# Optimization experiments

Hardware: AMD Instinct MI355X
Metric: run time of the kernel (lower is better)

Reference implementation:

```python
import jax, jax.numpy as jnp
import numpy as np

S, B, IN, H, NLAYERS = 2048, 1024, 4, 4, 6  # 3 stacked nn.LSTM modules x num_layers=2 each


def setup_inputs() -> dict:
    key = jax.random.key(0)
    ks = jax.random.split(key, 7)
    scale = 1.0 / np.sqrt(H)  # PyTorch LSTM init range
    return {
        "x": jax.random.normal(ks[0], (S, B, IN), jnp.float32),
        "w_ih": jax.random.uniform(ks[1], (NLAYERS, 4 * H, H), jnp.float32, -scale, scale),
        "w_hh": jax.random.uniform(ks[2], (NLAYERS, 4 * H, H), jnp.float32, -scale, scale),
        "b_ih": jax.random.uniform(ks[3], (NLAYERS, 4 * H), jnp.float32, -scale, scale),
        "b_hh": jax.random.uniform(ks[4], (NLAYERS, 4 * H), jnp.float32, -scale, scale),
        "reg_w": jax.random.uniform(ks[5], (1, H), jnp.float32, -scale, scale),
        "reg_b": jax.random.uniform(ks[6], (1,), jnp.float32, -scale, scale),
    }


def _lstm_layer(x, w_ih, w_hh, b_ih, b_hh):
    # x: [S, B, H_in]; PyTorch gate order: input, forget, cell(g), output
    b = x.shape[1]
    pre = jnp.einsum('sbi,gi->sbg', x, w_ih) + b_ih + b_hh  # [S, B, 4H], input projection hoisted out of scan

    def step(carry, p):
        h, c = carry
        gates = p + h @ w_hh.T
        i, f, g, o = jnp.split(gates, 4, axis=-1)
        c = jax.nn.sigmoid(f) * c + jax.nn.sigmoid(i) * jnp.tanh(g)
        h = jax.nn.sigmoid(o) * jnpat(c) if False else jax.nn.sigmoid(o) * jnp.tanh(c)
        return (h, c), h

    h0 = jnp.zeros((b, H), x.dtype)
    (_, _), ys = jax.lax.scan(step, (h0, h0), pre)
    return ys  # [S, B, H]


def reference(x, w_ih, w_hh, b_ih, b_hh, reg_w, reg_b):
    # 6 stacked LSTM layers (lstm1: layers 0-1, lstm2: 2-3, lstm3: 4-5).
    # Dropout (p=0.02) between layers and dropout3 are identity in eval mode.
    y = x
    for l in range(NLAYERS):
        y = _lstm_layer(y, w_ih[l], w_hh[l], b_ih[l], b_hh[l])
    out = jnp.einsum('sbh,oh->sbo', y, reg_w) + reg_b  # linear head, [S, B, 1]
    return out
```

## Files before the change

### kernel.cpp

```cpp
#include <hip/hip_runtime.h>

#define S_LEN  2048
#define BATCH  1024
#define NL     6
#define CH     16

typedef float f32x2 __attribute__((ext_vector_type(2)));

__device__ __forceinline__ float fexp2(float x) { return __builtin_amdgcn_exp2f(x); }
__device__ __forceinline__ float frcp(float x)  { return __builtin_amdgcn_rcpf(x); }

template <int CTRL>
__device__ __forceinline__ float dppf(float v) {
    return __int_as_float(__builtin_amdgcn_update_dpp(
        0, __float_as_int(v), CTRL, 0xF, 0xF, true));
}
__device__ __forceinline__ float bpermf(int addr, float v) {
    return __int_as_float(__builtin_amdgcn_ds_bpermute(addr, __float_as_int(v)));
}
__device__ __forceinline__ float swz4(float v) {
    return __int_as_float(__builtin_amdgcn_ds_swizzle(__float_as_int(v), 0x101F));
}
__device__ __forceinline__ f32x2 pkfma(f32x2 a, f32x2 b, f32x2 c) {
    f32x2 d;
    asm("v_pk_fma_f32 %0, %1, %2, %3" : "=v"(d) : "v"(a), "v"(b), "v"(c));
    return d;
}

__global__ __launch_bounds__(64, 1) void lstm_wavepipe(
    const float* __restrict__ x, const float* __restrict__ w_ih,
    const float* __restrict__ w_hh, const float* __restrict__ b_ih,
    const float* __restrict__ b_hh, const float* __restrict__ reg_w,
    const float* __restrict__ reg_b, float* __restrict__ out) {
    const int lane = threadIdx.x;
    const int L    = lane >> 3;
    const int q    = lane & 7;
    const int u    = q >> 1;
    const bool pOdd = (lane & 1);
    const int b    = blockIdx.x;
    const bool isFeeder = (L == 7);
    const bool isOut    = (lane == 48);

    const float KGc = -2.885390082f;
    const float KIc = -1.442695041f;

    f32x2 A1[4], A2[4], PB;
    if (L < NL) {
        const int gLo = pOdd ? 2 : 0;
        const int gHi = pOdd ? 3 : 1;
        const float klo = pOdd ? KGc : KIc;
        const float khi = KIc;
        const int rowLo = L * 16 + gLo * 4 + u;
        const int rowHi = L * 16 + gHi * 4 + u;
#pragma unroll
        for (int m = 0; m < 4; ++m) {
            const int cm = u ^ m;
            f32x2 a1, a2;
            a1.x = w_hh[rowLo * 4 + cm] * klo;
            a1.y = w_ih[rowHi * 4 + cm] * khi;
            a2.x = w_hh[rowHi * 4 + cm] * khi;
            a2.y = w_ih[rowLo * 4 + cm] * klo;
            A1[m] = a1; A2[m] = a2;
        }
        PB.x = (b_ih[rowLo] + b_hh[rowLo]) * klo;
        PB.y = (b_ih[rowHi] + b_hh[rowHi]) * khi;
    } else if (L == 6) {
#pragma unroll
        for (int m = 0; m < 4; ++m) {
            f32x2 a1; a1.x = 0.0f; a1.y = reg_w[u ^ m];
            A1[m] = a1;
            f32x2 a2; a2.x = 0.0f; a2.y = 0.0f;
            A2[m] = a2;
        }
        PB.x = 0.0f; PB.y = reg_b[0];
    } else {
#pragma unroll
        for (int m = 0; m < 4; ++m) {
            f32x2 z; z.x = 0.0f; z.y = 0.0f;
            A1[m] = z; A2[m] = z;
        }
        PB.x = 0.0f; PB.y = 0.0f;
    }
    const float aLo = pOdd ? 2.0f : 1.0f;
    const float bLo = pOdd ? -1.0f : 0.0f;
    f32x2 Z2; Z2.x = 0.0f; Z2.y = 0.0f;

    const int src   = (lane >= 8) ? (lane - 8) : (lane + 56);
    const int addrA = src << 2;
    const int addrB = (src ^ 4) << 2;

    float c = 0.0f;
    float bufP[CH], bufQ[CH], su[CH];
    const uint32_t xcol = (uint32_t)(b * 4 + u);
    uint32_t wi = xcol;
#pragma unroll
    for (int uu = 0; uu < CH; ++uu) { bufP[uu] = x[wi]; wi += 4096; }

    f32x2 P0, P2;
    {
        const float h0 = isFeeder ? bufP[0] : 0.0f;
        P0.x = h0; P0.y = bpermf(addrA, h0);
        P2.x = swz4(h0); P2.y = bpermf(addrB, h0);
    }

#define STEP(u_, NXV_, MASKF_) do {                                            \
    f32x2 P1, P3;                                                              \
    P1.x = dppf<0x4E>(P0.x); P1.y = dppf<0x4E>(P0.y);                          \
    P3.x = dppf<0x4E>(P2.x); P3.y = dppf<0x4E>(P2.y);                          \
    f32x2 C1 = pkfma(A1[0], P0, PB);                                           \
    f32x2 C2 = pkfma(A2[0], P0, Z2);                                           \
    C1 = pkfma(A1[1], P1, C1); C2 = pkfma(A2[1], P1, C2);                      \
    C1 = pkfma(A1[2], P2, C1); C2 = pkfma(A2[2], P2, C2);                      \
    C1 = pkfma(A1[3], P3, C1); C2 = pkfma(A2[3], P3, C2);                      \
    const float gLo = C1.x + C2.y;                                             \
    const float gHi = C1.y + C2.x;                                             \
    const float rA = frcp(1.0f + fexp2(gLo));                                  \
    const float rB = frcp(1.0f + fexp2(gHi));                                  \
    const float sA = fmaf(aLo, rA, bLo);       \
    const float tg = dppf<0xB1>(sA);                    \
    const float so = dppf<0xB1>(rB);                    \
    const float cn = fmaf(rB, c, sA * tg);             \
    const float th = fmaf(2.0f, frcp(1.0f + fexp2(cn * KGc)), -1.0f);          \
    const float hn = so * th;                                                  \
    const float hx = dppf<0xB1>(hn);                     \
    float hsel = pOdd ? hx : hn;                                               \
    if (MASKF_) {                                                              \
        const bool act = (u_ >= L);                    \
        c = act ? cn : c;                                                      \
        hsel = act ? hsel : P0.x;                                              \
    } else { c = cn; }                                                         \
    su[u_] = gHi;                                 \
    const float hpub = isFeeder ? (NXV_) : hsel;                               \
    P0.x = hpub;                                                               \
    P0.y = bpermf(addrA, hpub);                     \
    P2.x = swz4(hpub);                              \
    P2.y = bpermf(addrB, hpub);                     \
} while (0)

#define RUN_CHUNK(cc_, cur_, nxt_, MASKF_, PREFM_, GUARDF_, NSTEPS_) do {      \
    if ((PREFM_) == 1) {                                                       \
        _Pragma("unroll")                                                      \
        for (int uu = 0; uu < CH; ++uu) { nxt_[uu] = x[wi]; wi += 4096; }      \
    } else if ((PREFM_) == 2) {                                                \
        const float xl = x[2047u * 4096u + xcol];                              \
        _Pragma("unroll")                                                      \
        for (int uu = 0; uu < CH; ++uu) nxt_[uu] = xl;                         \
    }                                                                          \
    _Pragma("unroll")                                                          \
    for (int uu = 0; uu < (NSTEPS_); ++uu) {                                   \
        if (uu < CH - 1) STEP(uu, cur_[uu + 1], MASKF_);                       \
        else             STEP(uu, nxt_[0],      MASKF_);                       \
    }                                                                          \
    if (isOut) {                                                               \
        const int base = (cc_) * CH - 6;       \
        _Pragma("unroll")                                                      \
        for (int uu = 0; uu < (NSTEPS_); ++uu) {                               \
            const int t = base + uu;                                           \
            if (!(GUARDF_) || ((t >= 0) && (t < S_LEN)))                       \
                out[(size_t)t * BATCH + b] = su[uu];                           \
        }                                                                      \
    }                                                                          \
} while (0)

    RUN_CHUNK(0, bufP, bufQ, 1, 1, 1, CH);
#pragma unroll 1
    for (int cc = 1; cc < 127; cc += 2) {
        RUN_CHUNK(cc,     bufQ, bufP, 0, 1, 0, CH);
        RUN_CHUNK(cc + 1, bufP, bufQ, 0, 1, 0, CH);
    }
    RUN_CHUNK(127, bufQ, bufP, 0, 2, 0, CH);
    RUN_CHUNK(128, bufP, bufQ, 0, 0, 0, 6);
#undef RUN_CHUNK
#undef STEP
}

extern "C" void kernel_launch(void* const* d_in, const int* in_sizes, int n_in,
                              void* d_out, int out_size, void* d_ws, size_t ws_size,
                              hipStream_t stream) {
    const float* x     = (const float*)d_in[0];
    const float* w_ih  = (const float*)d_in[1];
    const float* w_hh  = (const float*)d_in[2];
    const float* b_ih  = (const float*)d_in[3];
    const float* b_hh  = (const float*)d_in[4];
    const float* reg_w = (const float*)d_in[5];
    const float* reg_b = (const float*)d_in[6];
    float* out = (float*)d_out;

    dim3 grid(BATCH);
    dim3 block(64);
    hipLaunchKernelGGL(lstm_wavepipe, grid, block, 0, stream, x, w_ih, w_hh,
                       b_ih, b_hh, reg_w, reg_b, out);
}
```

Measured before the change: 340.6 us.

## Deepen LSTM wavefront pipeline to two-step inter-layer lag with split h/c publish

Restructures the per-step recurrence so that each layer's hidden state reaches the next layer through one bpermute with a two-step lag, instead of a single-step lag that needed two bpermutes and a swizzle on the critical path. Own-layer h feeds the recurrence directly, and the cross-lane values for the next step are prefetched one step ahead. The KGc scale is folded into the cell state. The pipeline latency per layer doubles (12 drain steps instead of 6), and the output index offset and masking are adjusted to match. The aim is to shorten the serial dependency chain per timestep at the cost of a longer fill and drain.

```diff
diff --git a/kernel.cpp b/kernel.cpp
--- a/kernel.cpp
+++ b/kernel.cpp
@@ -81,30 +81,30 @@
         }
         PB.x = 0.0f; PB.y = 0.0f;
     }
-    const float aLo = pOdd ? 2.0f : 1.0f;
+    const float aLo = pOdd ? 2.0f : KGc;
     const float bLo = pOdd ? -1.0f : 0.0f;
     f32x2 Z2; Z2.x = 0.0f; Z2.y = 0.0f;
 
-    const int src   = (lane >= 8) ? (lane - 8) : (lane + 56);
-    const int addrA = src << 2;
-    const int addrB = (src ^ 4) << 2;
+    const int addrA = (((lane >= 8) ? (lane - 8) : (lane + 56)) << 2);
 
-    float c = 0.0f;
+    float h = 0.0f, cp = 0.0f;
     float bufP[CH], bufQ[CH], su[CH];
     const uint32_t xcol = (uint32_t)(b * 4 + u);
     uint32_t wi = xcol;
 #pragma unroll
     for (int uu = 0; uu < CH; ++uu) { bufP[uu] = x[wi]; wi += 4096; }
 
-    f32x2 P0, P2;
-    {
-        const float h0 = isFeeder ? bufP[0] : 0.0f;
-        P0.x = h0; P0.y = bpermf(addrA, h0);
-        P2.x = swz4(h0); P2.y = bpermf(addrB, h0);
-    }
+    const float pub0 = isFeeder ? bufP[0] : 0.0f;
+    const float pub1 = isFeeder ? bufP[1] : 0.0f;
+    float hupC = bpermf(addrA, pub0);
+    float hupN = bpermf(addrA, pub1);
+    float P2xC = 0.0f;
+    float P2yC = swz4(hupC);
 
 #define STEP(u_, NXV_, MASKF_) do {                                            \
-    f32x2 P1, P3;                                                              \
+    f32x2 P0, P1, P2, P3;                                                      \
+    P0.x = h;    P0.y = hupC;                                                  \
+    P2.x = P2xC; P2.y = P2yC;                                                  \
     P1.x = dppf<0x4E>(P0.x); P1.y = dppf<0x4E>(P0.y);                          \
     P3.x = dppf<0x4E>(P2.x); P3.y = dppf<0x4E>(P2.y);                          \
     f32x2 C1 = pkfma(A1[0], P0, PB);                                           \
@@ -112,29 +112,34 @@
     C1 = pkfma(A1[1], P1, C1); C2 = pkfma(A2[1], P1, C2);                      \
     C1 = pkfma(A1[2], P2, C1); C2 = pkfma(A2[2], P2, C2);                      \
     C1 = pkfma(A1[3], P3, C1); C2 = pkfma(A2[3], P3, C2);                      \
+    const float P2yN_ = swz4(hupN);                \
     const float gLo = C1.x + C2.y;                                             \
     const float gHi = C1.y + C2.x;                                             \
     const float rA = frcp(1.0f + fexp2(gLo));                                  \
     const float rB = frcp(1.0f + fexp2(gHi));                                  \
-    const float sA = fmaf(aLo, rA, bLo);       \
-    const float tg = dppf<0xB1>(sA);                    \
-    const float so = dppf<0xB1>(rB);                    \
-    const float cn = fmaf(rB, c, sA * tg);             \
-    const float th = fmaf(2.0f, frcp(1.0f + fexp2(cn * KGc)), -1.0f);          \
-    const float hn = so * th;                                                  \
-    const float hx = dppf<0xB1>(hn);                     \
-    float hsel = pOdd ? hx : hn;                                               \
+    const float sA = fmaf(aLo, rA, bLo);         \
+    const float X  = dppf<0xB1>(sA);                                           \
+    const float Y  = dppf<0xB1>(rB);                                           \
+    const float fsel = pOdd ? Y : rB;            \
+    const float ssel = pOdd ? rB : Y;            \
+    const float prod = sA * X;                    \
+    const float cnp  = fmaf(fsel, cp, prod);              \
+    const float th   = fmaf(2.0f, frcp(1.0f + fexp2(cnp)), -1.0f);             \
+    const float hn   = ssel * th;                                              \
+    float hpost, cpost;                                                        \
     if (MASKF_) {                                                              \
-        const bool act = (u_ >= L);                    \
-        c = act ? cn : c;                                                      \
-        hsel = act ? hsel : P0.x;                                              \
-    } else { c = cn; }                                                         \
+        const bool act = (u_ >= 2 * L);         \
+        cpost = act ? cnp : cp;                                                \
+        hpost = act ? hn : h;                                                  \
+    } else { cpost = cnp; hpost = hn; }                                        \
+    cp = cpost;                                                                \
     su[u_] = gHi;                                 \
-    const float hpub = isFeeder ? (NXV_) : hsel;                               \
-    P0.x = hpub;                                                               \
-    P0.y = bpermf(addrA, hpub);                     \
-    P2.x = swz4(hpub);                              \
-    P2.y = bpermf(addrB, hpub);                     \
+    const float P2xN_ = swz4(hpost);              \
+    const float hpub  = isFeeder ? (NXV_) : hpost;                             \
+    const float hupN2 = bpermf(addrA, hpub);      \
+    h = hpost;                                                                 \
+    hupC = hupN; hupN = hupN2;                                                 \
+    P2xC = P2xN_; P2yC = P2yN_;                                                \
 } while (0)
 
 #define RUN_CHUNK(cc_, cur_, nxt_, MASKF_, PREFM_, GUARDF_, NSTEPS_) do {      \
@@ -148,11 +153,12 @@
     }                                                                          \
     _Pragma("unroll")                                                          \
     for (int uu = 0; uu < (NSTEPS_); ++uu) {                                   \
-        if (uu < CH - 1) STEP(uu, cur_[uu + 1], MASKF_);                       \
-        else             STEP(uu, nxt_[0],      MASKF_);                       \
+        if (uu < CH - 2)       STEP(uu, cur_[uu + 2], MASKF_);                 \
+        else if (uu == CH - 2) STEP(uu, nxt_[0],      MASKF_);                 \
+        else                   STEP(uu, nxt_[1],      MASKF_);                 \
     }                                                                          \
     if (isOut) {                                                               \
-        const int base = (cc_) * CH - 6;       \
+        const int base = (cc_) * CH - 12;     \
         _Pragma("unroll")                                                      \
         for (int uu = 0; uu < (NSTEPS_); ++uu) {                               \
             const int t = base + uu;                                           \
@@ -169,7 +175,7 @@
         RUN_CHUNK(cc + 1, bufP, bufQ, 0, 1, 0, CH);
     }
     RUN_CHUNK(127, bufQ, bufP, 0, 2, 0, CH);
-    RUN_CHUNK(128, bufP, bufQ, 0, 0, 0, 6);
+    RUN_CHUNK(128, bufP, bufQ, 0, 0, 0, 12);
 #undef RUN_CHUNK
 #undef STEP
 }
```

Result: no change. 343.5 us (+0.9%).
